# Kernel tuning notes

Measured on AMD Instinct MI355X. Metric: run time of the kernel, lower is better.

## Reference

```python
import jax, jax.numpy as jnp
import numpy as np

NEG_INF = -9e15
ALPHA = 0.2  # leaky_relu slope


def gat_layer(h, adj, e_feat, W, We, a_s, a_d, a_e, h_res):
    """Dense multi-head GAT layer with edge features.
    h: [B,N,Fin], adj: [B,N,N] (0/1), e_feat: [B,N,N,Ein]
    W: [H,Fin,Fout], We: [H,Ein,Eout], a_s/a_d: [H,Fout], a_e: [H,Eout]
    Returns head-averaged (x_prime [B,N,Fout], e_prime [B,N,N,Eout]).
    """
    Wh = jnp.einsum('bnf,hfo->bhno', h, W)            # [B,H,N,Fout]
    Me = jnp.einsum('bnmf,hfe->bhnme', e_feat, We)    # [B,H,N,N,Eout]
    s_src = jnp.einsum('bhno,ho->bhn', Wh, a_s)
    s_dst = jnp.einsum('bhno,ho->bhn', Wh, a_d)
    s_edge = jnp.einsum('bhnme,he->bhnm', Me, a_e)
    scores = jax.nn.leaky_relu(s_src[:, :, :, None] + s_dst[:, :, None, :] + s_edge, ALPHA)
    scores = jnp.where(adj[:, None, :, :] > 0, scores, NEG_INF)
    att = jax.nn.softmax(scores, axis=-1)             # [B,H,N,N]
    h_prime = jnp.einsum('bhnm,bhmo->bhno', att, Wh)
    h_prime = jax.nn.elu(h_prime) + h_res[:, None]    # concat=True -> elu; residual add
    e_prime = att[..., None] * Me                      # attention-modulated edge features
    return h_prime.mean(axis=1), e_prime.mean(axis=1)


def setup_inputs() -> dict:
    key = jax.random.key(0)
    ks = jax.random.split(key, 16)
    B, N, F, E, H = 2, 256, 768, 7, 2
    nhid, ehid = 768, 768 // 2
    sc = lambda fan: 1.0 / np.sqrt(fan)
    return {
        'x': jax.random.normal(ks[0], (B, N, F), jnp.float32),
        'adj': jax.random.randint(ks[1], (B, N, N), 0, 2, jnp.int32),
        'e': jax.random.uniform(ks[2], (B, N, N, E), jnp.float32),
        'W1': jax.random.normal(ks[3], (H, F, nhid), jnp.float32) * sc(F),
        'We1': jax.random.normal(ks[4], (H, E, ehid), jnp.float32) * sc(E),
        'a1s': jax.random.normal(ks[5], (H, nhid), jnp.float32) * sc(nhid),
        'a1d': jax.random.normal(ks[6], (H, nhid), jnp.float32) * sc(nhid),
        'a1e': jax.random.normal(ks[7], (H, ehid), jnp.float32) * sc(ehid),
        'W2': jax.random.normal(ks[8], (H, nhid, nhid), jnp.float32) * sc(nhid),
        'We2': jax.random.normal(ks[9], (H, ehid, ehid), jnp.float32) * sc(ehid),
        'a2s': jax.random.normal(ks[10], (H, nhid), jnp.float32) * sc(nhid),
        'a2d': jax.random.normal(ks[11], (H, nhid), jnp.float32) * sc(nhid),
        'a2e': jax.random.normal(ks[12], (H, ehid), jnp.float32) * sc(ehid),
    }


def reference(x, adj, e, W1, We1, a1s, a1d, a1e, W2, We2, a2s, a2d, a2e):
    # dropout layers are identity in eval mode
    x1, e1 = gat_layer(x, adj, e, W1, We1, a1s, a1d, a1e, x)
    x2, e2 = gat_layer(x1, adj, e1, W2, We2, a2s, a2d, a2e, x)
    return x2, e2
```

## Files before the change

### kernel.cpp

```cpp
#include <hip/hip_runtime.h>
#include <hip/hip_bf16.h>
#include <cstddef>


typedef __attribute__((ext_vector_type(8))) short bf16x8;
typedef __attribute__((ext_vector_type(4))) short bf16x4;
typedef __attribute__((ext_vector_type(4))) float f32x4;
typedef unsigned short us;

#define DEVINL static __device__ __forceinline__

DEVINL us f2bf(float f) {
    union { float f; unsigned u; } v; v.f = f;
    return (us)((v.u + 0x7FFFu + ((v.u >> 16) & 1u)) >> 16);
}
DEVINL float bf2f(us b) {
    union { unsigned u; float f; } v; v.u = ((unsigned)b) << 16; return v.f;
}
DEVINL float wredmax(float v) {
#pragma unroll
    for (int s = 32; s; s >>= 1) v = fmaxf(v, __shfl_xor(v, s));
    return v;
}
DEVINL float wredsum(float v) {
#pragma unroll
    for (int s = 32; s; s >>= 1) v += __shfl_xor(v, s);
    return v;
}

DEVINL void transpose_body(const float* __restrict__ W, us* __restrict__ WT, int bb) {
    __shared__ us tile[64][65];
    const int ft = (bb % 12) * 64, ot = ((bb / 12) % 12) * 64, h = bb / 144;
    const int t = threadIdx.x;
    const float* Wh = W + (size_t)h * 589824;
    us* WTh = WT + (size_t)h * 589824;
#pragma unroll
    for (int i = 0; i < 16; i++) {
        int idx = t + i * 256, r = idx >> 6, c = idx & 63;
        tile[c][r] = f2bf(Wh[(size_t)(ft + r) * 768 + ot + c]);
    }
    __syncthreads();
#pragma unroll
    for (int i = 0; i < 2; i++) {
        int idx = t + i * 256, r = idx >> 3, c0 = (idx & 7) * 8;
        us pk[8];
#pragma unroll
        for (int j = 0; j < 8; j++) pk[j] = tile[r][c0 + j];
        *(bf16x8*)&WTh[(size_t)(ot + r) * 768 + ft + c0] = *(bf16x8*)pk;
    }
}

DEVINL void mcat_body(const float* __restrict__ We1, const float* __restrict__ We2,
                      float* __restrict__ Mcat, int h2, int tct) {
    __shared__ float we1L[16][384];
    __shared__ float part[16][128];
    const int t = threadIdx.x;
    for (int i = t; i < 6144; i += 256) {
        int m = i / 384, o = i % 384;
        int h1 = m >> 3, kk = m & 7;
        we1L[m][o] = (kk < 7) ? We1[(h1 * 7 + kk) * 384 + o] : 0.0f;
    }
    __syncthreads();
    const int tc = tct * 128 + (t & 127);
    const int half = t >> 7;
    float acc[16];
#pragma unroll
    for (int m = 0; m < 16; m++) acc[m] = 0.0f;
    const float* w2 = We2 + (size_t)h2 * 147456 + tc;
    for (int o = half * 192; o < half * 192 + 192; o++) {
        float wv = w2[(size_t)o * 384];
#pragma unroll
        for (int m = 0; m < 16; m++) acc[m] += we1L[m][o] * wv;
    }
    if (half == 1)
#pragma unroll
        for (int m = 0; m < 16; m++) part[m][t & 127] = acc[m];
    __syncthreads();
    if (half == 0) {
#pragma unroll
        for (int m = 0; m < 16; m++) {
            float v = 0.25f * (acc[m] + part[m][t]);
            int h1 = m >> 3, kk = m & 7;
            Mcat[((h1 * 2 + h2) * 8 + kk) * 384 + tc] = v;
        }
    }
}

DEVINL void pre_qu_body(const float* __restrict__ W1, const float* __restrict__ W2,
                        const float* __restrict__ We1,
                        const float* __restrict__ a1s, const float* __restrict__ a1d,
                        const float* __restrict__ a1e, const float* __restrict__ a2s,
                        const float* __restrict__ a2d,
                        float* __restrict__ q, float* __restrict__ u1, int blk) {
    const int g = blk * 32 + (threadIdx.x >> 3);
    const int lane = threadIdx.x & 7;
    float acc = 0.0f;
    if (g < 6144) {
        int vec = g / 1536, rem = g % 1536, h = rem / 768, f = rem % 768;
        const float* W = (vec < 2) ? W1 : W2;
        const float* a = (vec == 0) ? a1s : (vec == 1) ? a1d : (vec == 2) ? a2s : a2d;
        const float* wr = W + (size_t)(h * 768 + f) * 768;
        const float* ar = a + h * 768;
        for (int o = lane; o < 768; o += 8) acc += wr[o] * ar[o];
        for (int s = 4; s; s >>= 1) acc += __shfl_down(acc, s, 8);
        if (lane == 0) q[g] = acc;
    } else if (g < 6160) {
        int g2 = g - 6144, h = g2 >> 3, k = g2 & 7;
        if (k < 7) {
            const float* wr = We1 + (h * 7 + k) * 384;
            const float* ar = a1e + h * 384;
            for (int o = lane; o < 384; o += 8) acc += wr[o] * ar[o];
        }
        for (int s = 4; s; s >>= 1) acc += __shfl_down(acc, s, 8);
        if (lane == 0) u1[g2] = acc;
    }
}

DEVINL void cvt_body(const float* __restrict__ in, us* __restrict__ out, int blk) {
    int i = (blk * 256 + threadIdx.x) * 8;
    float4 v0 = *(const float4*)&in[i];
    float4 v1 = *(const float4*)&in[i + 4];
    us pk[8] = {f2bf(v0.x), f2bf(v0.y), f2bf(v0.z), f2bf(v0.w),
                f2bf(v1.x), f2bf(v1.y), f2bf(v1.z), f2bf(v1.w)};
    *(bf16x8*)&out[i] = *(bf16x8*)pk;
}

DEVINL void wcalc_body(const float* __restrict__ Mcat, const float* __restrict__ a2e,
                       float* __restrict__ w) {
    const int t = threadIdx.x, g = t >> 3, lane = t & 7;
    int hh = g >> 3, k = g & 7, h2 = hh & 1;
    float acc = 0.0f;
    if (k < 7)
        for (int o = lane; o < 384; o += 8) acc += Mcat[(hh * 8 + k) * 384 + o] * a2e[h2 * 384 + o];
    for (int s = 4; s; s >>= 1) acc += __shfl_down(acc, s, 8);
    if (lane == 0) w[g] = 2.0f * acc;
}

DEVINL void bfrag_body(const float* __restrict__ Mcat, us* __restrict__ Bfrag, int ct) {
    const int l = threadIdx.x;
    if (l < 64) {
        us pk[8];
#pragma unroll
        for (int j = 0; j < 8; j++)
            pk[j] = f2bf(Mcat[((l >> 4) * 8 + j) * 384 + ct * 16 + (l & 15)]);
        *(bf16x8*)&Bfrag[(ct * 64 + l) * 8] = *(bf16x8*)pk;
    }
}

DEVINL void sdots_body(const float* __restrict__ x, const float* __restrict__ qs,
                       const float* __restrict__ qd, float* __restrict__ out_s,
                       float* __restrict__ out_d, int n, int b) {
    const int t = threadIdx.x, wv = t >> 6;
    const float* xr = x + (size_t)(b * 256 + n) * 768;
    float a0 = 0, a1 = 0, a2 = 0, a3 = 0;
#pragma unroll
    for (int i = 0; i < 3; i++) {
        int k = i * 256 + t;
        float xv = xr[k];
        a0 += xv * qs[k];
        a1 += xv * qs[768 + k];
        a2 += xv * qd[k];
        a3 += xv * qd[768 + k];
    }
    a0 = wredsum(a0); a1 = wredsum(a1); a2 = wredsum(a2); a3 = wredsum(a3);
    __shared__ float part[4][4];
    if ((t & 63) == 0) { part[wv][0] = a0; part[wv][1] = a1; part[wv][2] = a2; part[wv][3] = a3; }
    __syncthreads();
    if (t == 0) {
        float r0 = 0, r1 = 0, r2 = 0, r3 = 0;
#pragma unroll
        for (int i = 0; i < 4; i++) { r0 += part[i][0]; r1 += part[i][1]; r2 += part[i][2]; r3 += part[i][3]; }
        out_s[(b * 2 + 0) * 256 + n] = r0;
        out_s[(b * 2 + 1) * 256 + n] = r1;
        out_d[(b * 2 + 0) * 256 + n] = r2;
        out_d[(b * 2 + 1) * 256 + n] = r3;
    }
}

DEVINL void att1_body(const float* __restrict__ e, const int* __restrict__ adj,
                      const float* __restrict__ s_s, const float* __restrict__ s_d,
                      const float* __restrict__ u1, us* __restrict__ attb,
                      int n, int bb) {
    __shared__ float eL[1792];
    __shared__ float smax[2][4], ssum[2][4];
    const int t = threadIdx.x, wv = t >> 6;
    const float* erow = e + (size_t)(bb * 256 + n) * 1792;
#pragma unroll
    for (int i = 0; i < 7; i++) eL[t + i * 256] = erow[t + i * 256];
    __syncthreads();
    float ss0 = s_s[(bb * 2 + 0) * 256 + n], ss1 = s_s[(bb * 2 + 1) * 256 + n];
    float sd0 = s_d[(bb * 2 + 0) * 256 + t], sd1 = s_d[(bb * 2 + 1) * 256 + t];
    float se0 = 0, se1 = 0;
#pragma unroll
    for (int k = 0; k < 7; k++) {
        float ev = eL[t * 7 + k];
        se0 += ev * u1[k];
        se1 += ev * u1[8 + k];
    }
    float sc0 = ss0 + sd0 + se0, sc1 = ss1 + sd1 + se1;
    sc0 = sc0 > 0.0f ? sc0 : 0.2f * sc0;
    sc1 = sc1 > 0.0f ? sc1 : 0.2f * sc1;
    bool ok = adj[(size_t)(bb * 256 + n) * 256 + t] > 0;
    sc0 = ok ? sc0 : -9e15f;
    sc1 = ok ? sc1 : -9e15f;
    float w0 = wredmax(sc0), w1 = wredmax(sc1);
    if ((t & 63) == 0) { smax[0][wv] = w0; smax[1][wv] = w1; }
    __syncthreads();
    float mx0 = fmaxf(fmaxf(smax[0][0], smax[0][1]), fmaxf(smax[0][2], smax[0][3]));
    float mx1 = fmaxf(fmaxf(smax[1][0], smax[1][1]), fmaxf(smax[1][2], smax[1][3]));
    float ex0 = __expf(sc0 - mx0), ex1 = __expf(sc1 - mx1);
    float su0 = wredsum(ex0), su1 = wredsum(ex1);
    if ((t & 63) == 0) { ssum[0][wv] = su0; ssum[1][wv] = su1; }
    __syncthreads();
    float i0 = 1.0f / (ssum[0][0] + ssum[0][1] + ssum[0][2] + ssum[0][3]);
    float i1 = 1.0f / (ssum[1][0] + ssum[1][1] + ssum[1][2] + ssum[1][3]);
    attb[((size_t)(bb * 2 + 0) * 256 + n) * 256 + t] = f2bf(ex0 * i0);
    attb[((size_t)(bb * 2 + 1) * 256 + n) * 256 + t] = f2bf(ex1 * i1);
}

DEVINL void gemm_xw_body(const us* __restrict__ A, const us* __restrict__ BT,
                         us* __restrict__ WhT, int mt, int ot, int h) {
    const int t = threadIdx.x, wv = t >> 6, l = t & 63;
    const int wm = wv >> 1, wn = wv & 1, lr = l & 15, lk = l >> 4;
    __shared__ us As[64][40];
    __shared__ us Bs[64][40];
    const int arow = t >> 2, acol = (t & 3) * 8;
    const us* Bh = BT + (size_t)h * 589824;
    f32x4 acc[2][2];
#pragma unroll
    for (int i = 0; i < 2; i++)
#pragma unroll
        for (int j = 0; j < 2; j++) acc[i][j] = (f32x4){0, 0, 0, 0};
    for (int k0 = 0; k0 < 768; k0 += 32) {
        __syncthreads();
        *(bf16x8*)&As[arow][acol] = *(const bf16x8*)&A[(size_t)(mt * 64 + arow) * 768 + k0 + acol];
        *(bf16x8*)&Bs[arow][acol] = *(const bf16x8*)&Bh[(size_t)(ot * 64 + arow) * 768 + k0 + acol];
        __syncthreads();
        bf16x8 af[2], bfv[2];
#pragma unroll
        for (int i = 0; i < 2; i++) af[i] = *(const bf16x8*)&As[wm * 32 + i * 16 + lr][lk * 8];
#pragma unroll
        for (int j = 0; j < 2; j++) bfv[j] = *(const bf16x8*)&Bs[wn * 32 + j * 16 + lr][lk * 8];
#pragma unroll
        for (int i = 0; i < 2; i++)
#pragma unroll
            for (int j = 0; j < 2; j++)
                acc[i][j] = __builtin_amdgcn_mfma_f32_16x16x32_bf16(af[i], bfv[j], acc[i][j], 0, 0, 0);
    }
#pragma unroll
    for (int i = 0; i < 2; i++)
#pragma unroll
        for (int j = 0; j < 2; j++) {
            int n0 = mt * 64 + wm * 32 + i * 16 + lk * 4;
            int og = ot * 64 + wn * 32 + j * 16 + lr;
            int b = n0 >> 8, n = n0 & 255;
            us pk[4];
#pragma unroll
            for (int r = 0; r < 4; r++) pk[r] = f2bf(acc[i][j][r]);
            *(bf16x4*)&WhT[((size_t)(b * 2 + h) * 768 + og) * 256 + n] = *(bf16x4*)pk;
        }
}

DEVINL void gemm_att_body(const us* __restrict__ attb, const us* __restrict__ WhT,
                          const float* __restrict__ resid, float* __restrict__ xout,
                          us* __restrict__ xbout, int mt, int ot, int b) {
    const int t = threadIdx.x, wv = t >> 6, l = t & 63;
    const int wm = wv >> 1, wn = wv & 1, lr = l & 15, lk = l >> 4;
    __shared__ us As2[32][40];
    __shared__ us Bs2[64][40];
    float res[2][4] = {};
    for (int h = 0; h < 2; h++) {
        const us* Ah = attb + (size_t)(b * 2 + h) * 65536;
        const us* Bh = WhT + (size_t)(b * 2 + h) * 196608;
        f32x4 acc[2];
        acc[0] = (f32x4){0, 0, 0, 0};
        acc[1] = (f32x4){0, 0, 0, 0};
        for (int k0 = 0; k0 < 256; k0 += 32) {
            __syncthreads();
            if (t < 128) {
                int ar = t >> 2, ac = (t & 3) * 8;
                *(bf16x8*)&As2[ar][ac] = *(const bf16x8*)&Ah[(size_t)(mt * 32 + ar) * 256 + k0 + ac];
            }
            {
                int br = t >> 2, bc = (t & 3) * 8;
                *(bf16x8*)&Bs2[br][bc] = *(const bf16x8*)&Bh[(size_t)(ot * 64 + br) * 256 + k0 + bc];
            }
            __syncthreads();
            bf16x8 af = *(const bf16x8*)&As2[wm * 16 + lr][lk * 8];
#pragma unroll
            for (int j = 0; j < 2; j++) {
                bf16x8 bv = *(const bf16x8*)&Bs2[wn * 32 + j * 16 + lr][lk * 8];
                acc[j] = __builtin_amdgcn_mfma_f32_16x16x32_bf16(af, bv, acc[j], 0, 0, 0);
            }
        }
#pragma unroll
        for (int j = 0; j < 2; j++)
#pragma unroll
            for (int r = 0; r < 4; r++) {
                float v = acc[j][r];
                res[j][r] += (v > 0.0f ? v : (expf(v) - 1.0f));
            }
        __syncthreads();
    }
#pragma unroll
    for (int j = 0; j < 2; j++) {
        int n0 = mt * 32 + wm * 16 + lk * 4;
        int og = ot * 64 + wn * 32 + j * 16 + lr;
#pragma unroll
        for (int r = 0; r < 4; r++) {
            size_t idx = (size_t)(b * 256 + n0 + r) * 768 + og;
            float v = 0.5f * res[j][r] + resid[idx];
            if (xout) xout[idx] = v;
            if (xbout) xbout[idx] = f2bf(v);
        }
    }
}

union Smem6 {
    struct {
        us    blB[1536 * 8];
        float eL[1792];
        float aL1[2][256];
        float aL2[2][256];
        float smax[2][4];
        float ssum[2][4];
    } a;
    struct {
        us aA[2][32][264];
        us Bs2[64][40];
    } b;
};

DEVINL void att2e2_body(const float* __restrict__ e, const int* __restrict__ adj,
                        const float* __restrict__ s_s, const float* __restrict__ s_d,
                        const float* __restrict__ w, const us* __restrict__ att1b,
                        const us* __restrict__ Bfrag, float* __restrict__ e2out,
                        Smem6& sm, int bb, int n) {
    const int t = threadIdx.x, wv4 = t >> 6;
    for (int i = t; i < 1536; i += 256)
        *(bf16x8*)&sm.a.blB[i * 8] = *(const bf16x8*)&Bfrag[(size_t)i * 8];
    const float* erow = e + (size_t)(bb * 256 + n) * 1792;
#pragma unroll
    for (int i = 0; i < 7; i++) sm.a.eL[t + i * 256] = erow[t + i * 256];
    const size_t a1base = (size_t)bb * 131072 + n * 256;
    float a10 = bf2f(att1b[a1base + t]);
    float a11 = bf2f(att1b[a1base + 65536 + t]);
    sm.a.aL1[0][t] = a10;
    sm.a.aL1[1][t] = a11;
    __syncthreads();
    float ss0 = s_s[(bb * 2 + 0) * 256 + n], ss1 = s_s[(bb * 2 + 1) * 256 + n];
    float sd0 = s_d[(bb * 2 + 0) * 256 + t], sd1 = s_d[(bb * 2 + 1) * 256 + t];
    float ew00 = 0, ew01 = 0, ew10 = 0, ew11 = 0;
#pragma unroll
    for (int k = 0; k < 7; k++) {
        float ev = sm.a.eL[t * 7 + k];
        ew00 += ev * w[k];
        ew01 += ev * w[8 + k];
        ew10 += ev * w[16 + k];
        ew11 += ev * w[24 + k];
    }
    float sc0 = ss0 + sd0 + a10 * ew00 + a11 * ew10;
    float sc1 = ss1 + sd1 + a10 * ew01 + a11 * ew11;
    sc0 = sc0 > 0.0f ? sc0 : 0.2f * sc0;
    sc1 = sc1 > 0.0f ? sc1 : 0.2f * sc1;
    bool ok = adj[(size_t)(bb * 256 + n) * 256 + t] > 0;
    sc0 = ok ? sc0 : -9e15f;
    sc1 = ok ? sc1 : -9e15f;
    float w0 = wredmax(sc0), w1 = wredmax(sc1);
    if ((t & 63) == 0) { sm.a.smax[0][wv4] = w0; sm.a.smax[1][wv4] = w1; }
    __syncthreads();
    float mx0 = fmaxf(fmaxf(sm.a.smax[0][0], sm.a.smax[0][1]), fmaxf(sm.a.smax[0][2], sm.a.smax[0][3]));
    float mx1 = fmaxf(fmaxf(sm.a.smax[1][0], sm.a.smax[1][1]), fmaxf(sm.a.smax[1][2], sm.a.smax[1][3]));
    float ex0 = __expf(sc0 - mx0), ex1 = __expf(sc1 - mx1);
    float su0 = wredsum(ex0), su1 = wredsum(ex1);
    if ((t & 63) == 0) { sm.a.ssum[0][wv4] = su0; sm.a.ssum[1][wv4] = su1; }
    __syncthreads();
    float i0 = 1.0f / (sm.a.ssum[0][0] + sm.a.ssum[0][1] + sm.a.ssum[0][2] + sm.a.ssum[0][3]);
    float i1 = 1.0f / (sm.a.ssum[1][0] + sm.a.ssum[1][1] + sm.a.ssum[1][2] + sm.a.ssum[1][3]);
    sm.a.aL2[0][t] = ex0 * i0;
    sm.a.aL2[1][t] = ex1 * i1;
    __syncthreads();
    const int wv = t >> 6, l = t & 63, le = l & 15, lq = l >> 4;
    const int h1 = lq >> 1, h2 = lq & 1;
    bf16x8 av[4];
#pragma unroll
    for (int g = 0; g < 4; g++) {
        int m = g * 64 + wv * 16 + le;
        float c = sm.a.aL1[h1][m] * sm.a.aL2[h2][m];
        us pk[8];
#pragma unroll
        for (int j = 0; j < 7; j++) pk[j] = f2bf(c * sm.a.eL[m * 7 + j]);
        pk[7] = 0;
        av[g] = *(bf16x8*)pk;
    }
    const f32x4 zero = {0, 0, 0, 0};
    const size_t rowbase = (size_t)bb * 65536 + n * 256;
#pragma unroll
    for (int cg = 0; cg < 3; cg++) {
        bf16x8 bfr[8];
#pragma unroll
        for (int i = 0; i < 8; i++) bfr[i] = *(const bf16x8*)&sm.a.blB[(cg * 512 + i * 64 + l) * 8];
        for (int g = 0; g < 4; g++) {
            size_t eidx = rowbase + g * 64 + wv * 16 + le;
#pragma unroll
            for (int i = 0; i < 8; i++) {
                f32x4 acc = __builtin_amdgcn_mfma_f32_16x16x32_bf16(bfr[i], av[g], zero, 0, 0, 0);
                *(f32x4*)&e2out[eidx * 384 + cg * 128 + i * 16 + lq * 4] = acc;
            }
        }
    }
}

DEVINL void gemm_att2_fat(const float* __restrict__ e, const int* __restrict__ adj,
                          const float* __restrict__ s2s, const float* __restrict__ s2d,
                          const float* __restrict__ wbuf, const us* __restrict__ att1b,
                          const us* __restrict__ WhT2, const float* __restrict__ resid,
                          float* __restrict__ x2out, Smem6& sm, int mt, int ot, int b) {
    const int t = threadIdx.x, wv = t >> 6, l = t & 63;
    for (int rr = 0; rr < 8; rr++) {
        const int r = wv * 8 + rr, n = mt * 32 + r, m0 = l * 4;
        const float* ep = e + ((size_t)(b * 256 + n) * 256 + m0) * 7;
        float ev[4][7];
#pragma unroll
        for (int mm = 0; mm < 4; mm++)
#pragma unroll
            for (int k = 0; k < 7; k++) ev[mm][k] = ep[mm * 7 + k];
        const int* adjp = adj + (size_t)(b * 256 + n) * 256 + m0;
        float ss0 = s2s[(b * 2 + 0) * 256 + n], ss1 = s2s[(b * 2 + 1) * 256 + n];
        float sc0[4], sc1[4];
#pragma unroll
        for (int mm = 0; mm < 4; mm++) {
            int m = m0 + mm;
            float sd0 = s2d[(b * 2 + 0) * 256 + m];
            float sd1 = s2d[(b * 2 + 1) * 256 + m];
            float a10 = bf2f(att1b[((size_t)(b * 2 + 0) * 256 + n) * 256 + m]);
            float a11 = bf2f(att1b[((size_t)(b * 2 + 1) * 256 + n) * 256 + m]);
            float ew00 = 0, ew01 = 0, ew10 = 0, ew11 = 0;
#pragma unroll
            for (int k = 0; k < 7; k++) {
                float evk = ev[mm][k];
                ew00 += evk * wbuf[k];
                ew01 += evk * wbuf[8 + k];
                ew10 += evk * wbuf[16 + k];
                ew11 += evk * wbuf[24 + k];
            }
            float s0 = ss0 + sd0 + a10 * ew00 + a11 * ew10;
            float s1 = ss1 + sd1 + a10 * ew01 + a11 * ew11;
            s0 = s0 > 0.0f ? s0 : 0.2f * s0;
            s1 = s1 > 0.0f ? s1 : 0.2f * s1;
            bool ok = adjp[mm] > 0;
            sc0[mm] = ok ? s0 : -9e15f;
            sc1[mm] = ok ? s1 : -9e15f;
        }
        float mx0 = fmaxf(fmaxf(sc0[0], sc0[1]), fmaxf(sc0[2], sc0[3]));
        float mx1 = fmaxf(fmaxf(sc1[0], sc1[1]), fmaxf(sc1[2], sc1[3]));
        mx0 = wredmax(mx0); mx1 = wredmax(mx1);
        float ex0[4], ex1[4], su0 = 0, su1 = 0;
#pragma unroll
        for (int mm = 0; mm < 4; mm++) {
            ex0[mm] = __expf(sc0[mm] - mx0); su0 += ex0[mm];
            ex1[mm] = __expf(sc1[mm] - mx1); su1 += ex1[mm];
        }
        su0 = wredsum(su0); su1 = wredsum(su1);
        float i0 = 1.0f / su0, i1 = 1.0f / su1;
        us p0[4], p1[4];
#pragma unroll
        for (int mm = 0; mm < 4; mm++) { p0[mm] = f2bf(ex0[mm] * i0); p1[mm] = f2bf(ex1[mm] * i1); }
        *(bf16x4*)&sm.b.aA[0][r][m0] = *(bf16x4*)p0;
        *(bf16x4*)&sm.b.aA[1][r][m0] = *(bf16x4*)p1;
    }
    __syncthreads();
    const int wm = wv >> 1, wn = wv & 1, lr = l & 15, lk = l >> 4;
    float res[2][4] = {};
    for (int h = 0; h < 2; h++) {
        const us* Bh = WhT2 + (size_t)(b * 2 + h) * 196608;
        f32x4 acc[2];
        acc[0] = (f32x4){0, 0, 0, 0};
        acc[1] = (f32x4){0, 0, 0, 0};
        for (int k0 = 0; k0 < 256; k0 += 32) {
            __syncthreads();
            {
                int br = t >> 2, bc = (t & 3) * 8;
                *(bf16x8*)&sm.b.Bs2[br][bc] = *(const bf16x8*)&Bh[(size_t)(ot * 64 + br) * 256 + k0 + bc];
            }
            __syncthreads();
            bf16x8 af = *(const bf16x8*)&sm.b.aA[h][wm * 16 + lr][k0 + lk * 8];
#pragma unroll
            for (int j = 0; j < 2; j++) {
                bf16x8 bv = *(const bf16x8*)&sm.b.Bs2[wn * 32 + j * 16 + lr][lk * 8];
                acc[j] = __builtin_amdgcn_mfma_f32_16x16x32_bf16(af, bv, acc[j], 0, 0, 0);
            }
        }
#pragma unroll
        for (int j = 0; j < 2; j++)
#pragma unroll
            for (int r = 0; r < 4; r++) {
                float v = acc[j][r];
                res[j][r] += (v > 0.0f ? v : (expf(v) - 1.0f));
            }
        __syncthreads();
    }
#pragma unroll
    for (int j = 0; j < 2; j++) {
        int n0 = mt * 32 + wm * 16 + lk * 4;
        int og = ot * 64 + wn * 32 + j * 16 + lr;
#pragma unroll
        for (int r = 0; r < 4; r++) {
            size_t idx = (size_t)(b * 256 + n0 + r) * 768 + og;
            x2out[idx] = 0.5f * res[j][r] + resid[idx];
        }
    }
}

__global__ __launch_bounds__(256) void stage1(
    const float* W1, const float* W2, const float* We1, const float* We2,
    const float* a1s, const float* a1d, const float* a1e,
    const float* a2s, const float* a2d, const float* x,
    us* W1T, us* W2T, us* xb, float* q, float* u1, float* Mcat) {
    int b = blockIdx.x;
    if (b < 6)          mcat_body(We1, We2, Mcat, b & 1, b >> 1);
    else if (b < 199)   pre_qu_body(W1, W2, We1, a1s, a1d, a1e, a2s, a2d, q, u1, b - 6);
    else if (b < 487)   transpose_body(W1, W1T, b - 199);
    else if (b < 775)   transpose_body(W2, W2T, b - 487);
    else                cvt_body(x, xb, b - 775);
}

__global__ __launch_bounds__(256) void stage2(
    const float* Mcat, const float* a2e, float* wbuf, us* Bfrag,
    const float* x, const float* qs, const float* qd, float* s1s, float* s1d) {
    int b = blockIdx.x;
    if (b < 1)        wcalc_body(Mcat, a2e, wbuf);
    else if (b < 25)  bfrag_body(Mcat, Bfrag, b - 1);
    else { int i = b - 25; sdots_body(x, qs, qd, s1s, s1d, i & 255, i >> 8); }
}

__global__ __launch_bounds__(256) void stage3(
    const float* e, const int* adj, const float* s1s, const float* s1d,
    const float* u1, us* att1b, const us* xb, const us* W1T, us* WhT1) {
    int b = blockIdx.x;
    if (b < 512) att1_body(e, adj, s1s, s1d, u1, att1b, b & 255, b >> 8);
    else { int g = b - 512; gemm_xw_body(xb, W1T, WhT1, g & 7, (g >> 3) % 12, g / 96); }
}

__global__ __launch_bounds__(256) void stage4(
    const us* att1b, const us* WhT1, const float* x, float* x1, us* xb1) {
    int b = blockIdx.x;
    gemm_att_body(att1b, WhT1, x, x1, xb1, b & 7, (b >> 3) % 12, b / 96);
}

__global__ __launch_bounds__(256) void stage5(
    const float* x1, const float* qs, const float* qd, float* s2s, float* s2d,
    const us* xb1, const us* W2T, us* WhT2) {
    int b = blockIdx.x;
    if (b < 512) sdots_body(x1, qs, qd, s2s, s2d, b & 255, b >> 8);
    else { int g = b - 512; gemm_xw_body(xb1, W2T, WhT2, g & 7, (g >> 3) % 12, g / 96); }
}

__global__ __launch_bounds__(256) void stage6(
    const float* e, const int* adj, const float* s2s, const float* s2d,
    const float* wbuf, const us* att1b, const us* Bfrag, float* e2out,
    const us* WhT2, const float* x, float* x2out) {
    __shared__ Smem6 sm;
    int b = blockIdx.x;
    if (b < 192) {
        int bb = b & 1, mt = (b >> 1) & 7, ot = b >> 4;
        gemm_att2_fat(e, adj, s2s, s2d, wbuf, att1b, WhT2, x, x2out, sm, mt, ot, bb);
    } else {
        int r = b - 192;
        att2e2_body(e, adj, s2s, s2d, wbuf, att1b, Bfrag, e2out, sm, r >> 8, r & 255);
    }
}

extern "C" void kernel_launch(void* const* d_in, const int* in_sizes, int n_in,
                              void* d_out, int out_size, void* d_ws, size_t ws_size,
                              hipStream_t stream) {
    const float* x   = (const float*)d_in[0];
    const int*   adj = (const int*)d_in[1];
    const float* e   = (const float*)d_in[2];
    const float* W1  = (const float*)d_in[3];
    const float* We1 = (const float*)d_in[4];
    const float* a1s = (const float*)d_in[5];
    const float* a1d = (const float*)d_in[6];
    const float* a1e = (const float*)d_in[7];
    const float* W2  = (const float*)d_in[8];
    const float* We2 = (const float*)d_in[9];
    const float* a2s = (const float*)d_in[10];
    const float* a2d = (const float*)d_in[11];
    const float* a2e = (const float*)d_in[12];

    float* out   = (float*)d_out;
    float* x2out = out;
    float* e2out = out + 393216;

    char* ws = (char*)d_ws;
    float* q     = (float*)(ws + 0);
    float* u1    = (float*)(ws + 24576);
    float* wbuf  = (float*)(ws + 24640);
    float* Mcat  = (float*)(ws + 24832);
    us*    Bfrag = (us*)(ws + 73984);
    float* s1s   = (float*)(ws + 98560);
    float* s1d   = (float*)(ws + 102656);
    float* s2s   = (float*)(ws + 106752);
    float* s2d   = (float*)(ws + 110848);
    us*    att1b = (us*)(ws + 114944);
    us*    W1T   = (us*)(ws + 1163520);
    us*    W2T   = (us*)(ws + 3522816);
    us*    xb    = (us*)(ws + 5882112);
    us*    xb1   = (us*)(ws + 6668544);
    us*    WhT1  = (us*)(ws + 7454976);
    us*    WhT2  = (us*)(ws + 9027840);
    float* x1    = (float*)(ws + 10600704);

    stage1<<<967, 256, 0, stream>>>(W1, W2, We1, We2, a1s, a1d, a1e, a2s, a2d,
                                    x, W1T, W2T, xb, q, u1, Mcat);
    stage2<<<537, 256, 0, stream>>>(Mcat, a2e, wbuf, Bfrag, x, q + 0, q + 1536, s1s, s1d);
    stage3<<<704, 256, 0, stream>>>(e, adj, s1s, s1d, u1, att1b, xb, W1T, WhT1);
    stage4<<<192, 256, 0, stream>>>(att1b, WhT1, x, x1, xb1);
    stage5<<<704, 256, 0, stream>>>(x1, q + 3072, q + 4608, s2s, s2d, xb1, W2T, WhT2);
    stage6<<<704, 256, 0, stream>>>(e, adj, s2s, s2d, wbuf, att1b, Bfrag, e2out,
                                    WhT2, x, x2out);
}
```

Baseline: 112.9 us.

## Fuse layer-1 attention softmax into att GEMM and fold layer-2 score dots into epilogue

Layer-1 attention softmax is now computed in each GEMM block and kept in shared memory, so the separate attention kernel and its reload of att from global memory go away. The epilogue accumulates the layer-2 source and destination score dot products with shared then global atomics, which removes the sdots pass over x1 and the x1 buffer. The xW1 GEMM moves into stage2, giving five launches instead of six. In exchange, each of the 12 output tiles per row block recomputes the softmax, adding redundant reads of e and adj, and the score sums need a zeroed buffer plus atomics, which makes summation order nondeterministic.

```diff
diff --git a/kernel.cpp b/kernel.cpp
--- a/kernel.cpp
+++ b/kernel.cpp
@@ -116,6 +116,10 @@
     }
 }
 
+DEVINL void zero_body(float* __restrict__ z) {
+    for (int i = threadIdx.x; i < 4096; i += 256) z[i] = 0.0f;
+}
+
 DEVINL void cvt_body(const float* __restrict__ in, us* __restrict__ out, int blk) {
     int i = (blk * 256 + threadIdx.x) * 8;
     float4 v0 = *(const float4*)&in[i];
@@ -177,47 +181,6 @@
     }
 }
 
-DEVINL void att1_body(const float* __restrict__ e, const int* __restrict__ adj,
-                      const float* __restrict__ s_s, const float* __restrict__ s_d,
-                      const float* __restrict__ u1, us* __restrict__ attb,
-                      int n, int bb) {
-    __shared__ float eL[1792];
-    __shared__ float smax[2][4], ssum[2][4];
-    const int t = threadIdx.x, wv = t >> 6;
-    const float* erow = e + (size_t)(bb * 256 + n) * 1792;
-#pragma unroll
-    for (int i = 0; i < 7; i++) eL[t + i * 256] = erow[t + i * 256];
-    __syncthreads();
-    float ss0 = s_s[(bb * 2 + 0) * 256 + n], ss1 = s_s[(bb * 2 + 1) * 256 + n];
-    float sd0 = s_d[(bb * 2 + 0) * 256 + t], sd1 = s_d[(bb * 2 + 1) * 256 + t];
-    float se0 = 0, se1 = 0;
-#pragma unroll
-    for (int k = 0; k < 7; k++) {
-        float ev = eL[t * 7 + k];
-        se0 += ev * u1[k];
-        se1 += ev * u1[8 + k];
-    }
-    float sc0 = ss0 + sd0 + se0, sc1 = ss1 + sd1 + se1;
-    sc0 = sc0 > 0.0f ? sc0 : 0.2f * sc0;
-    sc1 = sc1 > 0.0f ? sc1 : 0.2f * sc1;
-    bool ok = adj[(size_t)(bb * 256 + n) * 256 + t] > 0;
-    sc0 = ok ? sc0 : -9e15f;
-    sc1 = ok ? sc1 : -9e15f;
-    float w0 = wredmax(sc0), w1 = wredmax(sc1);
-    if ((t & 63) == 0) { smax[0][wv] = w0; smax[1][wv] = w1; }
-    __syncthreads();
-    float mx0 = fmaxf(fmaxf(smax[0][0], smax[0][1]), fmaxf(smax[0][2], smax[0][3]));
-    float mx1 = fmaxf(fmaxf(smax[1][0], smax[1][1]), fmaxf(smax[1][2], smax[1][3]));
-    float ex0 = __expf(sc0 - mx0), ex1 = __expf(sc1 - mx1);
-    float su0 = wredsum(ex0), su1 = wredsum(ex1);
-    if ((t & 63) == 0) { ssum[0][wv] = su0; ssum[1][wv] = su1; }
-    __syncthreads();
-    float i0 = 1.0f / (ssum[0][0] + ssum[0][1] + ssum[0][2] + ssum[0][3]);
-    float i1 = 1.0f / (ssum[1][0] + ssum[1][1] + ssum[1][2] + ssum[1][3]);
-    attb[((size_t)(bb * 2 + 0) * 256 + n) * 256 + t] = f2bf(ex0 * i0);
-    attb[((size_t)(bb * 2 + 1) * 256 + n) * 256 + t] = f2bf(ex1 * i1);
-}
-
 DEVINL void gemm_xw_body(const us* __restrict__ A, const us* __restrict__ BT,
                          us* __restrict__ WhT, int mt, int ot, int h) {
     const int t = threadIdx.x, wv = t >> 6, l = t & 63;
@@ -261,35 +224,92 @@
         }
 }
 
-DEVINL void gemm_att_body(const us* __restrict__ attb, const us* __restrict__ WhT,
-                          const float* __restrict__ resid, float* __restrict__ xout,
-                          us* __restrict__ xbout, int mt, int ot, int b) {
+struct Smem3 {
+    us    aA[2][32][264];
+    us    Bs2[64][40];
+    float sAcc[4][32];
+};
+
+DEVINL void fat_att_gemm1(const float* __restrict__ e, const int* __restrict__ adj,
+                          const float* __restrict__ s1s, const float* __restrict__ s1d,
+                          const float* __restrict__ u1, us* __restrict__ att1b,
+                          const us* __restrict__ WhT1, const float* __restrict__ resid,
+                          us* __restrict__ xb1, const float* __restrict__ q,
+                          float* __restrict__ s2s, float* __restrict__ s2d,
+                          Smem3& sm, int mt, int ot, int b) {
     const int t = threadIdx.x, wv = t >> 6, l = t & 63;
+    if (t < 128) ((float*)sm.sAcc)[t] = 0.0f;
+    for (int rr = 0; rr < 8; rr++) {
+        const int r = wv * 8 + rr, n = mt * 32 + r, m0 = l * 4;
+        const float* ep = e + ((size_t)(b * 256 + n) * 256 + m0) * 7;
+        float ev[4][7];
+#pragma unroll
+        for (int mm = 0; mm < 4; mm++)
+#pragma unroll
+            for (int k = 0; k < 7; k++) ev[mm][k] = ep[mm * 7 + k];
+        const int* adjp = adj + (size_t)(b * 256 + n) * 256 + m0;
+        float ss0 = s1s[(b * 2 + 0) * 256 + n], ss1 = s1s[(b * 2 + 1) * 256 + n];
+        float sc0[4], sc1[4];
+#pragma unroll
+        for (int mm = 0; mm < 4; mm++) {
+            int m = m0 + mm;
+            float sd0 = s1d[(b * 2 + 0) * 256 + m];
+            float sd1 = s1d[(b * 2 + 1) * 256 + m];
+            float se0 = 0, se1 = 0;
+#pragma unroll
+            for (int k = 0; k < 7; k++) {
+                float evk = ev[mm][k];
+                se0 += evk * u1[k];
+                se1 += evk * u1[8 + k];
+            }
+            float s0 = ss0 + sd0 + se0;
+            float s1 = ss1 + sd1 + se1;
+            s0 = s0 > 0.0f ? s0 : 0.2f * s0;
+            s1 = s1 > 0.0f ? s1 : 0.2f * s1;
+            bool ok = adjp[mm] > 0;
+            sc0[mm] = ok ? s0 : -9e15f;
+            sc1[mm] = ok ? s1 : -9e15f;
+        }
+        float mx0 = fmaxf(fmaxf(sc0[0], sc0[1]), fmaxf(sc0[2], sc0[3]));
+        float mx1 = fmaxf(fmaxf(sc1[0], sc1[1]), fmaxf(sc1[2], sc1[3]));
+        mx0 = wredmax(mx0); mx1 = wredmax(mx1);
+        float ex0[4], ex1[4], su0 = 0, su1 = 0;
+#pragma unroll
+        for (int mm = 0; mm < 4; mm++) {
+            ex0[mm] = __expf(sc0[mm] - mx0); su0 += ex0[mm];
+            ex1[mm] = __expf(sc1[mm] - mx1); su1 += ex1[mm];
+        }
+        su0 = wredsum(su0); su1 = wredsum(su1);
+        float i0 = 1.0f / su0, i1 = 1.0f / su1;
+        us p0[4], p1[4];
+#pragma unroll
+        for (int mm = 0; mm < 4; mm++) { p0[mm] = f2bf(ex0[mm] * i0); p1[mm] = f2bf(ex1[mm] * i1); }
+        *(bf16x4*)&sm.aA[0][r][m0] = *(bf16x4*)p0;
+        *(bf16x4*)&sm.aA[1][r][m0] = *(bf16x4*)p1;
+        if (ot == 0) {
+            *(bf16x4*)&att1b[((size_t)(b * 2 + 0) * 256 + n) * 256 + m0] = *(bf16x4*)p0;
+            *(bf16x4*)&att1b[((size_t)(b * 2 + 1) * 256 + n) * 256 + m0] = *(bf16x4*)p1;
+        }
+    }
+    __syncthreads();
     const int wm = wv >> 1, wn = wv & 1, lr = l & 15, lk = l >> 4;
-    __shared__ us As2[32][40];
-    __shared__ us Bs2[64][40];
     float res[2][4] = {};
     for (int h = 0; h < 2; h++) {
-        const us* Ah = attb + (size_t)(b * 2 + h) * 65536;
-        const us* Bh = WhT + (size_t)(b * 2 + h) * 196608;
+        const us* Bh = WhT1 + (size_t)(b * 2 + h) * 196608;
         f32x4 acc[2];
         acc[0] = (f32x4){0, 0, 0, 0};
         acc[1] = (f32x4){0, 0, 0, 0};
         for (int k0 = 0; k0 < 256; k0 += 32) {
             __syncthreads();
-            if (t < 128) {
-                int ar = t >> 2, ac = (t & 3) * 8;
-                *(bf16x8*)&As2[ar][ac] = *(const bf16x8*)&Ah[(size_t)(mt * 32 + ar) * 256 + k0 + ac];
-            }
             {
                 int br = t >> 2, bc = (t & 3) * 8;
-                *(bf16x8*)&Bs2[br][bc] = *(const bf16x8*)&Bh[(size_t)(ot * 64 + br) * 256 + k0 + bc];
+                *(bf16x8*)&sm.Bs2[br][bc] = *(const bf16x8*)&Bh[(size_t)(ot * 64 + br) * 256 + k0 + bc];
             }
             __syncthreads();
-            bf16x8 af = *(const bf16x8*)&As2[wm * 16 + lr][lk * 8];
+            bf16x8 af = *(const bf16x8*)&sm.aA[h][wm * 16 + lr][k0 + lk * 8];
 #pragma unroll
             for (int j = 0; j < 2; j++) {
-                bf16x8 bv = *(const bf16x8*)&Bs2[wn * 32 + j * 16 + lr][lk * 8];
+                bf16x8 bv = *(const bf16x8*)&sm.Bs2[wn * 32 + j * 16 + lr][lk * 8];
                 acc[j] = __builtin_amdgcn_mfma_f32_16x16x32_bf16(af, bv, acc[j], 0, 0, 0);
             }
         }
@@ -306,13 +326,28 @@
     for (int j = 0; j < 2; j++) {
         int n0 = mt * 32 + wm * 16 + lk * 4;
         int og = ot * 64 + wn * 32 + j * 16 + lr;
+        float qs0 = q[3072 + og], qs1 = q[3072 + 768 + og];
+        float qd0 = q[4608 + og], qd1 = q[4608 + 768 + og];
 #pragma unroll
         for (int r = 0; r < 4; r++) {
             size_t idx = (size_t)(b * 256 + n0 + r) * 768 + og;
             float v = 0.5f * res[j][r] + resid[idx];
-            if (xout) xout[idx] = v;
-            if (xbout) xbout[idx] = f2bf(v);
-        }
+            xb1[idx] = f2bf(v);
+            int row = wm * 16 + lk * 4 + r;
+            atomicAdd(&sm.sAcc[0][row], v * qs0);
+            atomicAdd(&sm.sAcc[1][row], v * qs1);
+            atomicAdd(&sm.sAcc[2][row], v * qd0);
+            atomicAdd(&sm.sAcc[3][row], v * qd1);
+        }
+    }
+    __syncthreads();
+    if (t < 128) {
+        int type = t >> 5, row = t & 31, n = mt * 32 + row;
+        float* dst = (type == 0) ? &s2s[(b * 2 + 0) * 256 + n]
+                   : (type == 1) ? &s2s[(b * 2 + 1) * 256 + n]
+                   : (type == 2) ? &s2d[(b * 2 + 0) * 256 + n]
+                                 : &s2d[(b * 2 + 1) * 256 + n];
+        atomicAdd(dst, sm.sAcc[type][row]);
     }
 }
 
@@ -516,47 +551,45 @@
     const float* W1, const float* W2, const float* We1, const float* We2,
     const float* a1s, const float* a1d, const float* a1e,
     const float* a2s, const float* a2d, const float* x,
-    us* W1T, us* W2T, us* xb, float* q, float* u1, float* Mcat) {
+    us* W1T, us* W2T, us* xb, float* q, float* u1, float* Mcat, float* sbufs) {
     int b = blockIdx.x;
     if (b < 6)          mcat_body(We1, We2, Mcat, b & 1, b >> 1);
     else if (b < 199)   pre_qu_body(W1, W2, We1, a1s, a1d, a1e, a2s, a2d, q, u1, b - 6);
     else if (b < 487)   transpose_body(W1, W1T, b - 199);
     else if (b < 775)   transpose_body(W2, W2T, b - 487);
-    else                cvt_body(x, xb, b - 775);
+    else if (b < 967)   cvt_body(x, xb, b - 775);
+    else                zero_body(sbufs);
 }
 
 __global__ __launch_bounds__(256) void stage2(
+    const us* xb, const us* W1T, us* WhT1,
     const float* Mcat, const float* a2e, float* wbuf, us* Bfrag,
     const float* x, const float* qs, const float* qd, float* s1s, float* s1d) {
     int b = blockIdx.x;
-    if (b < 1)        wcalc_body(Mcat, a2e, wbuf);
-    else if (b < 25)  bfrag_body(Mcat, Bfrag, b - 1);
-    else { int i = b - 25; sdots_body(x, qs, qd, s1s, s1d, i & 255, i >> 8); }
+    if (b < 192)      gemm_xw_body(xb, W1T, WhT1, b & 7, (b >> 3) % 12, b / 96);
+    else if (b < 704) { int i = b - 192; sdots_body(x, qs, qd, s1s, s1d, i & 255, i >> 8); }
+    else if (b == 704) wcalc_body(Mcat, a2e, wbuf);
+    else              bfrag_body(Mcat, Bfrag, b - 705);
 }
 
 __global__ __launch_bounds__(256) void stage3(
     const float* e, const int* adj, const float* s1s, const float* s1d,
-    const float* u1, us* att1b, const us* xb, const us* W1T, us* WhT1) {
+    const float* u1, us* att1b, const us* WhT1, const float* x, us* xb1,
+    const float* q, float* s2s, float* s2d) {
+    __shared__ Smem3 sm;
     int b = blockIdx.x;
-    if (b < 512) att1_body(e, adj, s1s, s1d, u1, att1b, b & 255, b >> 8);
-    else { int g = b - 512; gemm_xw_body(xb, W1T, WhT1, g & 7, (g >> 3) % 12, g / 96); }
+    int bb = b & 1, mt = (b >> 1) & 7, ot = b >> 4;
+    fat_att_gemm1(e, adj, s1s, s1d, u1, att1b, WhT1, x, xb1, q, s2s, s2d,
+                  sm, mt, ot, bb);
 }
 
 __global__ __launch_bounds__(256) void stage4(
-    const us* att1b, const us* WhT1, const float* x, float* x1, us* xb1) {
-    int b = blockIdx.x;
-    gemm_att_body(att1b, WhT1, x, x1, xb1, b & 7, (b >> 3) % 12, b / 96);
+    const us* xb1, const us* W2T, us* WhT2) {
+    int g = blockIdx.x;
+    gemm_xw_body(xb1, W2T, WhT2, g & 7, (g >> 3) % 12, g / 96);
 }
 
 __global__ __launch_bounds__(256) void stage5(
-    const float* x1, const float* qs, const float* qd, float* s2s, float* s2d,
-    const us* xb1, const us* W2T, us* WhT2) {
-    int b = blockIdx.x;
-    if (b < 512) sdots_body(x1, qs, qd, s2s, s2d, b & 255, b >> 8);
-    else { int g = b - 512; gemm_xw_body(xb1, W2T, WhT2, g & 7, (g >> 3) % 12, g / 96); }
-}
-
-__global__ __launch_bounds__(256) void stage6(
     const float* e, const int* adj, const float* s2s, const float* s2d,
     const float* wbuf, const us* att1b, const us* Bfrag, float* e2out,
     const us* WhT2, const float* x, float* x2out) {
@@ -609,14 +642,14 @@
     us*    xb1   = (us*)(ws + 6668544);
     us*    WhT1  = (us*)(ws + 7454976);
     us*    WhT2  = (us*)(ws + 9027840);
-    float* x1    = (float*)(ws + 10600704);
-
-    stage1<<<967, 256, 0, stream>>>(W1, W2, We1, We2, a1s, a1d, a1e, a2s, a2d,
-                                    x, W1T, W2T, xb, q, u1, Mcat);
-    stage2<<<537, 256, 0, stream>>>(Mcat, a2e, wbuf, Bfrag, x, q + 0, q + 1536, s1s, s1d);
-    stage3<<<704, 256, 0, stream>>>(e, adj, s1s, s1d, u1, att1b, xb, W1T, WhT1);
-    stage4<<<192, 256, 0, stream>>>(att1b, WhT1, x, x1, xb1);
-    stage5<<<704, 256, 0, stream>>>(x1, q + 3072, q + 4608, s2s, s2d, xb1, W2T, WhT2);
-    stage6<<<704, 256, 0, stream>>>(e, adj, s2s, s2d, wbuf, att1b, Bfrag, e2out,
+
+    stage1<<<968, 256, 0, stream>>>(W1, W2, We1, We2, a1s, a1d, a1e, a2s, a2d,
+                                    x, W1T, W2T, xb, q, u1, Mcat, s1s);
+    stage2<<<729, 256, 0, stream>>>(xb, W1T, WhT1, Mcat, a2e, wbuf, Bfrag,
+                                    x, q + 0, q + 1536, s1s, s1d);
+    stage3<<<192, 256, 0, stream>>>(e, adj, s1s, s1d, u1, att1b, WhT1, x, xb1,
+                                    q, s2s, s2d);
+    stage4<<<192, 256, 0, stream>>>(xb1, W2T, WhT2);
+    stage5<<<704, 256, 0, stream>>>(e, adj, s2s, s2d, wbuf, att1b, Bfrag, e2out,
                                     WhT2, x, x2out);
 }
```

After: 126.8 us. 12.3% more time.
